# Optimization experiments

Hardware: AMD Instinct MI355X
Metric: run time of the kernel (lower is better)

Reference implementation:

```python
import jax, jax.numpy as jnp
import numpy as np

B, T, C, U = 256, 512, 512, 512  # batch, timesteps, n_in, units


def setup_inputs() -> dict:
    key = jax.random.key(0)
    k1, k2, k3, k4 = jax.random.split(key, 4)
    x = jax.random.normal(k1, (B, T, C), dtype=jnp.float32)
    dones = (jax.random.uniform(k2, (B, T, 1)) < 0.05).astype(jnp.float32)
    # keras 'uniform' initializer default range is [-0.05, 0.05]
    wx = jax.random.uniform(k3, (C, 4 * U), jnp.float32, -0.05, 0.05)
    wh = jax.random.uniform(k4, (U, 4 * U), jnp.float32, -0.05, 0.05)
    b = jnp.zeros((4 * U,), jnp.float32)
    return {"x": x, "dones": dones, "wx": wx, "wh": wh, "b": b}


def reference(x, dones, wx, wh, b):
    # x: [B,T,C], dones: [B,T,1], wx: [C,4U], wh: [U,4U], b: [4U]
    Bn, Tn, Cn = x.shape
    Un = wh.shape[0]

    def step(carry, xt):
        c, h = carry                     # [B,U] each
        xi, dt = xt                      # xi: [B,C], dt: [B,1]
        keep = 1.0 - dt
        c = c * keep
        h = h * keep
        z = xi @ wx + h @ wh + b         # [B,4U]
        i, f, o, u = jnp.split(z, 4, axis=-1)
        i = jax.nn.sigmoid(i)
        f = jax.nn.sigmoid(f)
        o = jax.nn.sigmoid(o)
        u = jnp.tanh(u)
        c = f * c + i * u
        h = o * jnp.tanh(c)
        return (c, h), h

    c0 = jnp.zeros((Bn, Un), x.dtype)   # self.states starts at zeros
    h0 = jnp.zeros((Bn, Un), x.dtype)
    (c, h), hs = jax.lax.scan(step, (c0, h0), (x.transpose(1, 0, 2), dones.transpose(1, 0, 2)))
    xs = hs.transpose(1, 0, 2)          # [B,T,U] (return_sequence=True)
    s = jnp.concatenate([c, h], axis=-1)  # [B,2U] (squeezed final state)
    return xs, s
```

## Files before the change

### kernel.cpp

```cpp
#include <hip/hip_runtime.h>

#define BATCH 256
#define TT 512
#define CIN 512
#define UU 512
#define ZN 2048
#define BT (BATCH*TT)
#define NWGPB 16

typedef __attribute__((ext_vector_type(8))) short short8;
typedef __attribute__((ext_vector_type(4))) float f32x4;

__device__ __forceinline__ short f2bf(float f){
  unsigned u = __float_as_uint(f);
  u += 0x7fffu + ((u >> 16) & 1u);
  return (short)(u >> 16);
}
__device__ __forceinline__ float bf2f(unsigned short s){
  unsigned u = ((unsigned)s) << 16;
  return __uint_as_float(u);
}

#define GLD16(g, l) __builtin_amdgcn_global_load_lds( \
    (const __attribute__((address_space(1))) void*)(g), \
    (__attribute__((address_space(3))) void*)(l), 16, 0, 0)

#define CLOAD(dst, p, OFFSTR) asm volatile( \
    "global_load_dwordx4 %0, %1, off offset:" OFFSTR " sc0 sc1" \
    : "=v"(dst) : "v"(p) : "memory")
#define CLOADW(dst, p) asm volatile( \
    "global_load_dword %0, %1, off sc0 sc1" \
    : "=v"(dst) : "v"(p) : "memory")

__device__ __forceinline__ void st_coh_u16(void* p, unsigned v){
  asm volatile("global_store_short %0, %1, off sc0 sc1" :: "v"(p), "v"(v) : "memory");
}
__device__ __forceinline__ void st_coh_u32(void* p, unsigned v){
  asm volatile("global_store_dword %0, %1, off sc0 sc1" :: "v"(p), "v"(v) : "memory");
}

__device__ __forceinline__ float sigm(float x){ return 1.0f/(1.0f + __expf(-x)); }
__device__ __forceinline__ float tanh_fast(float x){ return 1.0f - 2.0f/(1.0f + __expf(2.0f*x)); }

__global__ __launch_bounds__(256) void convert_x_kernel(const float* __restrict__ x,
                                                        short* __restrict__ xb){
  const long total = (long)TT*BATCH*64;
  const long stride = (long)gridDim.x * blockDim.x;
  for (long i = (long)blockIdx.x * blockDim.x + threadIdx.x; i < total; i += stride){
    const int c8 = (int)(i & 63);
    const long tb = i >> 6;
    const int b = (int)(tb & (BATCH-1));
    const int t = (int)(tb >> 8);
    const float* src = x + ((long)b*TT + t)*CIN + c8*8;
    const float4 v0 = *(const float4*)(src);
    const float4 v1 = *(const float4*)(src + 4);
    short8 o;
    o[0]=f2bf(v0.x); o[1]=f2bf(v0.y); o[2]=f2bf(v0.z); o[3]=f2bf(v0.w);
    o[4]=f2bf(v1.x); o[5]=f2bf(v1.y); o[6]=f2bf(v1.z); o[7]=f2bf(v1.w);
    *(short8*)(xb + i*8) = o;
  }
}

__global__ __launch_bounds__(256) void transpose_w_kernel(
    const float* __restrict__ wx, const float* __restrict__ wh,
    short* __restrict__ wxt, short* __restrict__ wht){
  const float* src = blockIdx.z ? wh : wx;
  short* dst = blockIdx.z ? wht : wxt;
  __shared__ float tile[32][33];
  const int nt = blockIdx.x << 5;
  const int kt = blockIdx.y << 5;
  const int tx = threadIdx.x & 31, ty = threadIdx.x >> 5;
  #pragma unroll
  for (int i = 0; i < 32; i += 8)
    tile[ty+i][tx] = src[(long)(kt+ty+i)*ZN + nt+tx];
  __syncthreads();
  #pragma unroll
  for (int i = 0; i < 32; i += 8)
    dst[(long)(nt+ty+i)*512 + kt+tx] = f2bf(tile[tx][ty+i]);
}

__global__ __launch_bounds__(256) void gemm_xpart_kernel(
    const short* __restrict__ A, const short* __restrict__ Bt,
    const float* __restrict__ bias, short* __restrict__ Co){
  __shared__ short As[128*32];
  __shared__ short Bs[128*32];
  const int wg = blockIdx.x;
  const int xcd = wg & 7;
  const int ii = wg >> 3;
  const long m0 = (long)(xcd*128 + (ii >> 4)) << 7;
  const long n0 = (long)(ii & 15) << 7;
  const int tid = threadIdx.x;
  const int lane = tid & 63;
  const int wave = tid >> 6;
  const int wm = wave & 1, wn = wave >> 1;
  f32x4 acc[4][4] = {};
  const int srow = tid >> 2;
  const int sseg = tid & 3;
  const long aoff = (m0 + srow) * 512 + sseg * 8;
  const long boff = (n0 + srow) * 512 + sseg * 8;
  short* ldsa = &As[tid * 8];
  short* ldsb = &Bs[tid * 8];
  for (int k0 = 0; k0 < 512; k0 += 32){
    __syncthreads();
    GLD16(A + aoff + k0, ldsa);
    GLD16(A + aoff + 64*512 + k0, ldsa + 2048);
    GLD16(Bt + boff + k0, ldsb);
    GLD16(Bt + boff + 64*512 + k0, ldsb + 2048);
    __syncthreads();
    const int kb = (lane >> 4) * 8;
    short8 af[4], bf[4];
    #pragma unroll
    for (int mi = 0; mi < 4; mi++) af[mi] = *(const short8*)&As[(wm*64 + mi*16 + (lane&15))*32 + kb];
    #pragma unroll
    for (int ni = 0; ni < 4; ni++) bf[ni] = *(const short8*)&Bs[(wn*64 + ni*16 + (lane&15))*32 + kb];
    #pragma unroll
    for (int mi = 0; mi < 4; mi++)
      #pragma unroll
      for (int ni = 0; ni < 4; ni++)
        acc[mi][ni] = __builtin_amdgcn_mfma_f32_16x16x32_bf16(af[mi], bf[ni], acc[mi][ni], 0, 0, 0);
  }
  #pragma unroll
  for (int ni = 0; ni < 4; ni++){
    const long col = n0 + wn*64 + ni*16 + (lane & 15);
    const float bv = bias[col];
    #pragma unroll
    for (int mi = 0; mi < 4; mi++){
      const long row = m0 + wm*64 + mi*16 + ((lane >> 4) << 2);
      #pragma unroll
      for (int r = 0; r < 4; r++)
        Co[(row + r)*ZN + col] = f2bf(acc[mi][ni][r] + bv);
    }
  }
}

__global__ __launch_bounds__(512, 2) void lstm_persist_kernel(
    const short* __restrict__ xpart, const float* __restrict__ dones,
    const short* __restrict__ wht, short* __restrict__ hb0,
    short* __restrict__ hb1, unsigned* __restrict__ flags,
    float* __restrict__ out){
  __shared__ short h_lds[8192];
  __shared__ float zpart[128*19 + 16];
  const int tid = threadIdx.x;
  const int lane = tid & 63;
  const int wv = tid >> 6;
  const int bg = blockIdx.x & 15;
  const int cg = blockIdx.x >> 4;
  const int rb = bg << 4;
  const int uc = cg << 5;
  const int j = lane & 15;
  const int hq = lane >> 4;
  const int g_w = wv >> 1;
  const int ucl = ((wv & 1) << 4) + j;
  const int zl = g_w*32 + ucl;

  short8 bfr[16];
  {
    const short* wsrc = wht + ((long)(g_w*512 + uc + ucl))*512 + hq*8;
    #pragma unroll
    for (int m = 0; m < 16; m++)
      bfr[m] = *(const short8*)(wsrc + m*32);
  }

  const int srow = tid >> 5;
  const int scol = (tid & 31) << 4;
  const int swb = (srow << 10) + (scol << 1);
  const int sxor = (srow & 7) << 4;
  const int arb = (j << 10) + (hq << 4);
  const int axor = (j & 7) << 4;

  const int erow = tid >> 5;
  const int euj  = tid & 31;
  const int eucol = uc + euj;
  const int row  = rb + erow;

  unsigned* fl = flags + bg*16;
  const unsigned short* xp16 = (const unsigned short*)xpart;

  float c = 0.0f;
  float dn;
  unsigned short xp[4];
  dn = dones[(long)row*TT + 0];
  #pragma unroll
  for (int g = 0; g < 4; g++)
    xp[g] = xp16[((long)0*BATCH + row)*ZN + (g<<9) + eucol];

  for (int t = 0; t < TT; t++){
    {
      const short* hsrc = ((t & 1) ? hb1 : hb0) + (long)(rb + srow)*UU + scol;
      short8 hv0, hv1;
      CLOAD(hv0, hsrc, "0");
      CLOAD(hv1, hsrc, "16");
      asm volatile("s_waitcnt vmcnt(0)" ::: "memory");
      *(short8*)((char*)h_lds + ( swb       ^ sxor)) = hv0;
      *(short8*)((char*)h_lds + ((swb + 16) ^ sxor)) = hv1;
    }
    __syncthreads();
    short8 a[16];
    #pragma unroll
    for (int m = 0; m < 16; m++)
      a[m] = *(const short8*)((const char*)h_lds + ((arb + (m << 6)) ^ axor));
    f32x4 acc0 = {}, acc1 = {};
    #pragma unroll
    for (int m = 0; m < 16; m += 2){
      acc0 = __builtin_amdgcn_mfma_f32_16x16x32_bf16(a[m],   bfr[m],   acc0, 0, 0, 0);
      acc1 = __builtin_amdgcn_mfma_f32_16x16x32_bf16(a[m+1], bfr[m+1], acc1, 0, 0, 0);
    }
    const f32x4 acc = acc0 + acc1;
    #pragma unroll
    for (int r = 0; r < 4; r++)
      zpart[zl*19 + hq*4 + r] = acc[r];
    __syncthreads();
    const float keep = 1.0f - dn;
    const float cold = c * keep;
    const float z0 = bf2f(xp[0]) + keep*zpart[(0*32 + euj)*19 + erow];
    const float z1 = bf2f(xp[1]) + keep*zpart[(1*32 + euj)*19 + erow];
    const float z2 = bf2f(xp[2]) + keep*zpart[(2*32 + euj)*19 + erow];
    const float z3 = bf2f(xp[3]) + keep*zpart[(3*32 + euj)*19 + erow];
    const float gi = sigm(z0);
    const float gf = sigm(z1);
    const float go = sigm(z2);
    const float gu = tanh_fast(z3);
    const float cn = gf*cold + gi*gu;
    const float hn = go * tanh_fast(cn);
    c = cn;
    if (t == TT-1){
      out[(long)row*TT*UU + (long)t*UU + eucol] = hn;
      float* s = out + (long)BATCH*TT*UU;
      s[(long)row*2*UU + eucol] = cn;
      s[(long)row*2*UU + UU + eucol] = hn;
    } else {
      short* hdst = (t & 1) ? hb0 : hb1;
      st_coh_u16(hdst + (long)row*UU + eucol, (unsigned)(unsigned short)f2bf(hn));
      asm volatile("s_waitcnt vmcnt(0)" ::: "memory");
      __syncthreads();
      if (tid == 0) st_coh_u32(fl + cg, (unsigned)(t+1));
      out[(long)row*TT*UU + (long)t*UU + eucol] = hn;
      dn = dones[(long)row*TT + (t+1)];
      #pragma unroll
      for (int g = 0; g < 4; g++)
        xp[g] = xp16[((long)(t+1)*BATCH + row)*ZN + (g<<9) + eucol];
      if (wv == 0){
        const unsigned tgt = (unsigned)(t+1);
        unsigned v;
        for (;;){
          CLOADW(v, fl + (lane & 15));
          asm volatile("s_waitcnt vmcnt(0)" ::: "memory");
          if (__all((int)(v >= tgt))) break;
          __builtin_amdgcn_s_sleep(1);
        }
      }
      __syncthreads();
    }
  }
}

extern "C" void kernel_launch(void* const* d_in, const int* in_sizes, int n_in,
                              void* d_out, int out_size, void* d_ws, size_t ws_size,
                              hipStream_t stream){
  const float* x     = (const float*)d_in[0];
  const float* dones = (const float*)d_in[1];
  const float* wx    = (const float*)d_in[2];
  const float* wh    = (const float*)d_in[3];
  const float* b     = (const float*)d_in[4];
  float* out = (float*)d_out;
  char* ws = (char*)d_ws;
  short* x_tb  = (short*)(ws);
  short* wx_t  = (short*)(ws + 134217728L);
  short* wh_t  = (short*)(ws + 136314880L);
  short* xpart = (short*)(ws + 138412032L);
  short* hb0   = (short*)(ws + 675282944L);
  short* hb1   = (short*)(ws + 675545088L);
  unsigned* flags = (unsigned*)(ws + 675807232L);

  hipMemsetAsync(hb0, 0, 262144, stream);
  hipMemsetAsync(flags, 0, 1024, stream);
  convert_x_kernel<<<2048, 256, 0, stream>>>(x, x_tb);
  transpose_w_kernel<<<dim3(64,16,2), 256, 0, stream>>>(wx, wh, wx_t, wh_t);
  gemm_xpart_kernel<<<16384, 256, 0, stream>>>(x_tb, wx_t, b, xpart);
  lstm_persist_kernel<<<256, 512, 0, stream>>>(xpart, dones, wh_t, hb0, hb1, flags, out);
}
```

Measured before the change: 1.856 ms.

## Restructure persistent LSTM step to 4 waves with split-K and per-gate MFMA reuse

The recurrent kernel drops from 512 to 256 threads per workgroup. Each wave now holds weights for all four gates of 16 units over half of K, and reuses each loaded h fragment across four MFMAs. Partial sums from the K halves are exchanged through LDS, and each lane computes the cell update for two rows directly from its accumulators, so the padded transposed zpart shuffle is gone. This cuts LDS reads and the number of waves that sync per step, at the cost of more weight registers per thread and an unswizzled LDS layout that may cause bank conflicts.

```diff
diff --git a/kernel.cpp b/kernel.cpp
--- a/kernel.cpp
+++ b/kernel.cpp
@@ -6,7 +6,6 @@
 #define UU 512
 #define ZN 2048
 #define BT (BATCH*TT)
-#define NWGPB 16
 
 typedef __attribute__((ext_vector_type(8))) short short8;
 typedef __attribute__((ext_vector_type(4))) float f32x4;
@@ -133,117 +132,140 @@
   }
 }
 
-__global__ __launch_bounds__(512, 2) void lstm_persist_kernel(
+__global__ __launch_bounds__(256, 1) void lstm_persist_kernel(
     const short* __restrict__ xpart, const float* __restrict__ dones,
     const short* __restrict__ wht, short* __restrict__ hb0,
     short* __restrict__ hb1, unsigned* __restrict__ flags,
     float* __restrict__ out){
   __shared__ short h_lds[8192];
-  __shared__ float zpart[128*19 + 16];
+  __shared__ float zx[4096];
   const int tid = threadIdx.x;
-  const int lane = tid & 63;
+  const int l = tid & 63;
   const int wv = tid >> 6;
+  const int kh = wv & 1;
+  const int ug = wv >> 1;
   const int bg = blockIdx.x & 15;
   const int cg = blockIdx.x >> 4;
   const int rb = bg << 4;
-  const int uc = cg << 5;
-  const int j = lane & 15;
-  const int hq = lane >> 4;
-  const int g_w = wv >> 1;
-  const int ucl = ((wv & 1) << 4) + j;
-  const int zl = g_w*32 + ucl;
-
-  short8 bfr[16];
-  {
-    const short* wsrc = wht + ((long)(g_w*512 + uc + ucl))*512 + hq*8;
-    #pragma unroll
-    for (int m = 0; m < 16; m++)
-      bfr[m] = *(const short8*)(wsrc + m*32);
-  }
-
-  const int srow = tid >> 5;
-  const int scol = (tid & 31) << 4;
-  const int swb = (srow << 10) + (scol << 1);
-  const int sxor = (srow & 7) << 4;
-  const int arb = (j << 10) + (hq << 4);
-  const int axor = (j & 7) << 4;
-
-  const int erow = tid >> 5;
-  const int euj  = tid & 31;
-  const int eucol = uc + euj;
-  const int row  = rb + erow;
+  const int ucw = (cg << 5) + (ug << 4);
+  const int j = l & 15;
+  const int hq = l >> 4;
+
+  short8 bfr[4][8];
+  #pragma unroll
+  for (int g = 0; g < 4; g++){
+    const short* wsrc = wht + ((long)(g*512 + ucw + j))*512 + kh*256 + hq*8;
+    #pragma unroll
+    for (int m = 0; m < 8; m++)
+      bfr[g][m] = *(const short8*)(wsrc + m*32);
+  }
+
+  const int srow = tid & 15;
+  const int skg  = tid >> 4;
+  const long sgoff = (long)(rb + srow)*UU + skg*32;
+  short* sdst = h_lds + skg*512 + srow*8;
+
+  const int row0 = rb + hq*4 + kh*2;
+  const int ucol = ucw + j;
 
   unsigned* fl = flags + bg*16;
   const unsigned short* xp16 = (const unsigned short*)xpart;
 
-  float c = 0.0f;
-  float dn;
-  unsigned short xp[4];
-  dn = dones[(long)row*TT + 0];
-  #pragma unroll
-  for (int g = 0; g < 4; g++)
-    xp[g] = xp16[((long)0*BATCH + row)*ZN + (g<<9) + eucol];
+  float c0 = 0.f, c1 = 0.f;
+  float dn0, dn1;
+  unsigned short xp0[4], xp1[4];
+  dn0 = dones[(long)row0*TT];
+  dn1 = dones[(long)(row0+1)*TT];
+  #pragma unroll
+  for (int g = 0; g < 4; g++){
+    xp0[g] = xp16[(long)row0*ZN + (g<<9) + ucol];
+    xp1[g] = xp16[(long)(row0+1)*ZN + (g<<9) + ucol];
+  }
 
   for (int t = 0; t < TT; t++){
     {
-      const short* hsrc = ((t & 1) ? hb1 : hb0) + (long)(rb + srow)*UU + scol;
-      short8 hv0, hv1;
-      CLOAD(hv0, hsrc, "0");
-      CLOAD(hv1, hsrc, "16");
+      const short* hs = ((t & 1) ? hb1 : hb0) + sgoff;
+      short8 v0, v1, v2, v3;
+      CLOAD(v0, hs, "0"); CLOAD(v1, hs, "16"); CLOAD(v2, hs, "32"); CLOAD(v3, hs, "48");
       asm volatile("s_waitcnt vmcnt(0)" ::: "memory");
-      *(short8*)((char*)h_lds + ( swb       ^ sxor)) = hv0;
-      *(short8*)((char*)h_lds + ((swb + 16) ^ sxor)) = hv1;
+      *(short8*)(sdst      ) = v0;
+      *(short8*)(sdst + 128) = v1;
+      *(short8*)(sdst + 256) = v2;
+      *(short8*)(sdst + 384) = v3;
     }
     __syncthreads();
-    short8 a[16];
-    #pragma unroll
-    for (int m = 0; m < 16; m++)
-      a[m] = *(const short8*)((const char*)h_lds + ((arb + (m << 6)) ^ axor));
-    f32x4 acc0 = {}, acc1 = {};
-    #pragma unroll
-    for (int m = 0; m < 16; m += 2){
-      acc0 = __builtin_amdgcn_mfma_f32_16x16x32_bf16(a[m],   bfr[m],   acc0, 0, 0, 0);
-      acc1 = __builtin_amdgcn_mfma_f32_16x16x32_bf16(a[m+1], bfr[m+1], acc1, 0, 0, 0);
-    }
-    const f32x4 acc = acc0 + acc1;
-    #pragma unroll
-    for (int r = 0; r < 4; r++)
-      zpart[zl*19 + hq*4 + r] = acc[r];
+    f32x4 acc[4] = {};
+    const short* abase = h_lds + kh*4096 + l*8;
+    #pragma unroll
+    for (int m = 0; m < 8; m++){
+      const short8 a = *(const short8*)(abase + m*512);
+      #pragma unroll
+      for (int g = 0; g < 4; g++)
+        acc[g] = __builtin_amdgcn_mfma_f32_16x16x32_bf16(a, bfr[g][m], acc[g], 0, 0, 0);
+    }
+    #pragma unroll
+    for (int g = 0; g < 4; g++)
+      *(f32x4*)&zx[(wv*4 + g)*256 + l*4] = acc[g];
     __syncthreads();
-    const float keep = 1.0f - dn;
-    const float cold = c * keep;
-    const float z0 = bf2f(xp[0]) + keep*zpart[(0*32 + euj)*19 + erow];
-    const float z1 = bf2f(xp[1]) + keep*zpart[(1*32 + euj)*19 + erow];
-    const float z2 = bf2f(xp[2]) + keep*zpart[(2*32 + euj)*19 + erow];
-    const float z3 = bf2f(xp[3]) + keep*zpart[(3*32 + euj)*19 + erow];
-    const float gi = sigm(z0);
-    const float gf = sigm(z1);
-    const float go = sigm(z2);
-    const float gu = tanh_fast(z3);
-    const float cn = gf*cold + gi*gu;
-    const float hn = go * tanh_fast(cn);
-    c = cn;
+    const int pvb = (wv ^ 1)*4;
+    f32x4 pz[4];
+    #pragma unroll
+    for (int g = 0; g < 4; g++)
+      pz[g] = *(const f32x4*)&zx[(pvb + g)*256 + l*4];
+    float zs0[4], zs1[4];
+    #pragma unroll
+    for (int g = 0; g < 4; g++){
+      zs0[g] = kh ? (acc[g][2] + pz[g][2]) : (acc[g][0] + pz[g][0]);
+      zs1[g] = kh ? (acc[g][3] + pz[g][3]) : (acc[g][1] + pz[g][1]);
+    }
+    const float keep0 = 1.0f - dn0;
+    const float keep1 = 1.0f - dn1;
+    const float z00 = bf2f(xp0[0]) + keep0*zs0[0];
+    const float z01 = bf2f(xp0[1]) + keep0*zs0[1];
+    const float z02 = bf2f(xp0[2]) + keep0*zs0[2];
+    const float z03 = bf2f(xp0[3]) + keep0*zs0[3];
+    const float z10 = bf2f(xp1[0]) + keep1*zs1[0];
+    const float z11 = bf2f(xp1[1]) + keep1*zs1[1];
+    const float z12 = bf2f(xp1[2]) + keep1*zs1[2];
+    const float z13 = bf2f(xp1[3]) + keep1*zs1[3];
+    const float gi0 = sigm(z00), gf0 = sigm(z01), go0 = sigm(z02), gu0 = tanh_fast(z03);
+    const float gi1 = sigm(z10), gf1 = sigm(z11), go1 = sigm(z12), gu1 = tanh_fast(z13);
+    const float cn0 = gf0*(c0*keep0) + gi0*gu0;
+    const float cn1 = gf1*(c1*keep1) + gi1*gu1;
+    const float hn0 = go0 * tanh_fast(cn0);
+    const float hn1 = go1 * tanh_fast(cn1);
+    c0 = cn0; c1 = cn1;
+    const long ob0 = (long)row0*TT*UU + (long)t*UU + ucol;
     if (t == TT-1){
-      out[(long)row*TT*UU + (long)t*UU + eucol] = hn;
+      out[ob0] = hn0;
+      out[ob0 + (long)TT*UU] = hn1;
       float* s = out + (long)BATCH*TT*UU;
-      s[(long)row*2*UU + eucol] = cn;
-      s[(long)row*2*UU + UU + eucol] = hn;
+      s[(long)row0*2*UU + ucol] = cn0;
+      s[(long)row0*2*UU + UU + ucol] = hn0;
+      s[(long)(row0+1)*2*UU + ucol] = cn1;
+      s[(long)(row0+1)*2*UU + UU + ucol] = hn1;
     } else {
       short* hdst = (t & 1) ? hb0 : hb1;
-      st_coh_u16(hdst + (long)row*UU + eucol, (unsigned)(unsigned short)f2bf(hn));
+      st_coh_u16(hdst + (long)row0*UU + ucol, (unsigned)(unsigned short)f2bf(hn0));
+      st_coh_u16(hdst + (long)(row0+1)*UU + ucol, (unsigned)(unsigned short)f2bf(hn1));
       asm volatile("s_waitcnt vmcnt(0)" ::: "memory");
       __syncthreads();
       if (tid == 0) st_coh_u32(fl + cg, (unsigned)(t+1));
-      out[(long)row*TT*UU + (long)t*UU + eucol] = hn;
-      dn = dones[(long)row*TT + (t+1)];
+      out[ob0] = hn0;
+      out[ob0 + (long)TT*UU] = hn1;
+      dn0 = dones[(long)row0*TT + (t+1)];
+      dn1 = dones[(long)(row0+1)*TT + (t+1)];
+      const long xb = ((long)(t+1)*BATCH)*ZN + ucol;
       #pragma unroll
-      for (int g = 0; g < 4; g++)
-        xp[g] = xp16[((long)(t+1)*BATCH + row)*ZN + (g<<9) + eucol];
+      for (int g = 0; g < 4; g++){
+        xp0[g] = xp16[xb + (long)row0*ZN + (g<<9)];
+        xp1[g] = xp16[xb + (long)(row0+1)*ZN + (g<<9)];
+      }
       if (wv == 0){
         const unsigned tgt = (unsigned)(t+1);
         unsigned v;
         for (;;){
-          CLOADW(v, fl + (lane & 15));
+          CLOADW(v, fl + (l & 15));
           asm volatile("s_waitcnt vmcnt(0)" ::: "memory");
           if (__all((int)(v >= tgt))) break;
           __builtin_amdgcn_s_sleep(1);
@@ -277,5 +299,5 @@
   convert_x_kernel<<<2048, 256, 0, stream>>>(x, x_tb);
   transpose_w_kernel<<<dim3(64,16,2), 256, 0, stream>>>(wx, wh, wx_t, wh_t);
   gemm_xpart_kernel<<<16384, 256, 0, stream>>>(x_tb, wx_t, b, xpart);
-  lstm_persist_kernel<<<256, 512, 0, stream>>>(xpart, dones, wh_t, hb0, hb1, flags, out);
-}
+  lstm_persist_kernel<<<256, 256, 0, stream>>>(xpart, dones, wh_t, hb0, hb1, flags, out);
+}
```

After: 2.076 ms. +11.8%, slower.

## Split persistent LSTM across 512 smaller workgroups with 16-unit column slices

Applied to the files above, without the earlier changes.

Repartitions the persistent recurrent kernel from 256 workgroups of 512 threads (32 units each) to 512 workgroups of 256 threads (16 units each), so each batch group now synchronizes 32 workgroups instead of 16. The LDS layout for h is changed to a k-major, unswizzled arrangement that lets lanes read MFMA A-fragments directly, and the register prefetch of all 16 fragments is replaced with on-the-fly loads. This spreads the per-step work across more CUs to shorten the serial step latency, at the cost of a wider flag barrier, each block re-loading the full 16-row h tile for less compute, and possible LDS bank conflicts without the XOR swizzle.

```diff
diff --git a/kernel.cpp b/kernel.cpp
--- a/kernel.cpp
+++ b/kernel.cpp
@@ -6,7 +6,6 @@
 #define UU 512
 #define ZN 2048
 #define BT (BATCH*TT)
-#define NWGPB 16
 
 typedef __attribute__((ext_vector_type(8))) short short8;
 typedef __attribute__((ext_vector_type(4))) float f32x4;
@@ -133,89 +132,85 @@
   }
 }
 
-__global__ __launch_bounds__(512, 2) void lstm_persist_kernel(
+__global__ __launch_bounds__(256, 2) void lstm_persist_kernel(
     const short* __restrict__ xpart, const float* __restrict__ dones,
     const short* __restrict__ wht, short* __restrict__ hb0,
     short* __restrict__ hb1, unsigned* __restrict__ flags,
     float* __restrict__ out){
   __shared__ short h_lds[8192];
-  __shared__ float zpart[128*19 + 16];
+  __shared__ float zpart[64*19 + 16];
   const int tid = threadIdx.x;
-  const int lane = tid & 63;
+  const int l = tid & 63;
   const int wv = tid >> 6;
-  const int bg = blockIdx.x & 15;
-  const int cg = blockIdx.x >> 4;
+  const int bg = blockIdx.x >> 5;
+  const int cg = blockIdx.x & 31;
   const int rb = bg << 4;
-  const int uc = cg << 5;
-  const int j = lane & 15;
-  const int hq = lane >> 4;
-  const int g_w = wv >> 1;
-  const int ucl = ((wv & 1) << 4) + j;
-  const int zl = g_w*32 + ucl;
+  const int uc = cg << 4;
+  const int j = l & 15;
+  const int hq = l >> 4;
 
   short8 bfr[16];
   {
-    const short* wsrc = wht + ((long)(g_w*512 + uc + ucl))*512 + hq*8;
+    const short* wsrc = wht + ((long)(wv*512 + uc + j))*512 + hq*8;
     #pragma unroll
     for (int m = 0; m < 16; m++)
       bfr[m] = *(const short8*)(wsrc + m*32);
   }
 
-  const int srow = tid >> 5;
-  const int scol = (tid & 31) << 4;
-  const int swb = (srow << 10) + (scol << 1);
-  const int sxor = (srow & 7) << 4;
-  const int arb = (j << 10) + (hq << 4);
-  const int axor = (j & 7) << 4;
-
-  const int erow = tid >> 5;
-  const int euj  = tid & 31;
+  const int srow = tid & 15;
+  const int skg  = tid >> 4;
+  const long sgoff = (long)(rb + srow)*UU + skg*32;
+  short* sdst = h_lds + skg*512 + srow*8;
+
+  const int erow = tid >> 4;
+  const int euj  = tid & 15;
   const int eucol = uc + euj;
   const int row  = rb + erow;
 
-  unsigned* fl = flags + bg*16;
+  unsigned* fl = flags + bg*32;
   const unsigned short* xp16 = (const unsigned short*)xpart;
 
   float c = 0.0f;
   float dn;
   unsigned short xp[4];
-  dn = dones[(long)row*TT + 0];
+  dn = dones[(long)row*TT];
   #pragma unroll
   for (int g = 0; g < 4; g++)
-    xp[g] = xp16[((long)0*BATCH + row)*ZN + (g<<9) + eucol];
+    xp[g] = xp16[(long)row*ZN + (g<<9) + eucol];
 
   for (int t = 0; t < TT; t++){
     {
-      const short* hsrc = ((t & 1) ? hb1 : hb0) + (long)(rb + srow)*UU + scol;
-      short8 hv0, hv1;
-      CLOAD(hv0, hsrc, "0");
-      CLOAD(hv1, hsrc, "16");
+      const short* hs = ((t & 1) ? hb1 : hb0) + sgoff;
+      short8 v0, v1, v2, v3;
+      CLOAD(v0, hs, "0"); CLOAD(v1, hs, "16"); CLOAD(v2, hs, "32"); CLOAD(v3, hs, "48");
       asm volatile("s_waitcnt vmcnt(0)" ::: "memory");
-      *(short8*)((char*)h_lds + ( swb       ^ sxor)) = hv0;
-      *(short8*)((char*)h_lds + ((swb + 16) ^ sxor)) = hv1;
-    }
-    __syncthreads();
-    short8 a[16];
-    #pragma unroll
-    for (int m = 0; m < 16; m++)
-      a[m] = *(const short8*)((const char*)h_lds + ((arb + (m << 6)) ^ axor));
+      *(short8*)(sdst      ) = v0;
+      *(short8*)(sdst + 128) = v1;
+      *(short8*)(sdst + 256) = v2;
+      *(short8*)(sdst + 384) = v3;
+    }
+    __syncthreads();
+    const short* abase = h_lds + l*8;
     f32x4 acc0 = {}, acc1 = {};
     #pragma unroll
     for (int m = 0; m < 16; m += 2){
-      acc0 = __builtin_amdgcn_mfma_f32_16x16x32_bf16(a[m],   bfr[m],   acc0, 0, 0, 0);
-      acc1 = __builtin_amdgcn_mfma_f32_16x16x32_bf16(a[m+1], bfr[m+1], acc1, 0, 0, 0);
+      const short8 a0 = *(const short8*)(abase + m*512);
+      const short8 a1 = *(const short8*)(abase + m*512 + 512);
+      acc0 = __builtin_amdgcn_mfma_f32_16x16x32_bf16(a0, bfr[m],   acc0, 0, 0, 0);
+      acc1 = __builtin_amdgcn_mfma_f32_16x16x32_bf16(a1, bfr[m+1], acc1, 0, 0, 0);
     }
     const f32x4 acc = acc0 + acc1;
+    const int zl = wv*16 + j;
     #pragma unroll
     for (int r = 0; r < 4; r++)
       zpart[zl*19 + hq*4 + r] = acc[r];
     __syncthreads();
     const float keep = 1.0f - dn;
     const float cold = c * keep;
-    const float z0 = bf2f(xp[0]) + keep*zpart[(0*32 + euj)*19 + erow];
-    const float z1 = bf2f(xp[1]) + keep*zpart[(1*32 + euj)*19 + erow];
-    const float z2 = bf2f(xp[2]) + keep*zpart[(2*32 + euj)*19 + erow];
-    const float z3 = bf2f(xp[3]) + keep*zpart[(3*32 + euj)*19 + erow];
+    const float z0 = bf2f(xp[0]) + keep*zpart[(0*16 + euj)*19 + erow];
+    const float z1 = bf2f(xp[1]) + keep*zpart[(1*16 + euj)*19 + erow];
+    const float z2 = bf2f(xp[2]) + keep*zpart[(2*16 + euj)*19 + erow];
+    const float z3 = bf2f(xp[3]) + keep*zpart[(3*16 + euj)*19 + erow];
     const float gi = sigm(z0);
     const float gf = sigm(z1);
     const float go = sigm(z2);
@@ -236,14 +231,15 @@
       if (tid == 0) st_coh_u32(fl + cg, (unsigned)(t+1));
       out[(long)row*TT*UU + (long)t*UU + eucol] = hn;
       dn = dones[(long)row*TT + (t+1)];
+      const long xb = ((long)(t+1)*BATCH + row)*ZN + eucol;
       #pragma unroll
       for (int g = 0; g < 4; g++)
-        xp[g] = xp16[((long)(t+1)*BATCH + row)*ZN + (g<<9) + eucol];
+        xp[g] = xp16[xb + (g<<9)];
       if (wv == 0){
         const unsigned tgt = (unsigned)(t+1);
         unsigned v;
         for (;;){
-          CLOADW(v, fl + (lane & 15));
+          CLOADW(v, fl + (l & 31));
           asm volatile("s_waitcnt vmcnt(0)" ::: "memory");
           if (__all((int)(v >= tgt))) break;
           __builtin_amdgcn_s_sleep(1);
@@ -273,9 +269,9 @@
   unsigned* flags = (unsigned*)(ws + 675807232L);
 
   hipMemsetAsync(hb0, 0, 262144, stream);
-  hipMemsetAsync(flags, 0, 1024, stream);
+  hipMemsetAsync(flags, 0, 2048, stream);
   convert_x_kernel<<<2048, 256, 0, stream>>>(x, x_tb);
   transpose_w_kernel<<<dim3(64,16,2), 256, 0, stream>>>(wx, wh, wx_t, wh_t);
   gemm_xpart_kernel<<<16384, 256, 0, stream>>>(x_tb, wx_t, b, xpart);
-  lstm_persist_kernel<<<256, 512, 0, stream>>>(xpart, dones, wh_t, hb0, hb1, flags, out);
-}
+  lstm_persist_kernel<<<512, 256, 0, stream>>>(xpart, dones, wh_t, hb0, hb1, flags, out);
+}
```

Measured after the change: 2.715 ms. +46.3%, slower.

## Fuse x fp32-to-bf16 conversion into input GEMM and simplify h LDS layout

Applied to the files above, without the earlier changes.

Removes the separate convert_x kernel and has the input-projection GEMM read fp32 x directly, converting to bf16 while staging into LDS, which drops one full pass over x and the bf16 intermediate buffer. The GEMM's A-tile loads change from async global-to-LDS copies to register loads plus explicit LDS stores, which may add latency per k-step. The persistent LSTM kernel also reorganizes how h is staged in LDS so each lane reads its MFMA fragment with a simple linear offset, without the XOR swizzle and the up-front register array.

```diff
diff --git a/kernel.cpp b/kernel.cpp
--- a/kernel.cpp
+++ b/kernel.cpp
@@ -6,7 +6,6 @@
 #define UU 512
 #define ZN 2048
 #define BT (BATCH*TT)
-#define NWGPB 16
 
 typedef __attribute__((ext_vector_type(8))) short short8;
 typedef __attribute__((ext_vector_type(4))) float f32x4;
@@ -41,25 +40,6 @@
 
 __device__ __forceinline__ float sigm(float x){ return 1.0f/(1.0f + __expf(-x)); }
 __device__ __forceinline__ float tanh_fast(float x){ return 1.0f - 2.0f/(1.0f + __expf(2.0f*x)); }
-
-__global__ __launch_bounds__(256) void convert_x_kernel(const float* __restrict__ x,
-                                                        short* __restrict__ xb){
-  const long total = (long)TT*BATCH*64;
-  const long stride = (long)gridDim.x * blockDim.x;
-  for (long i = (long)blockIdx.x * blockDim.x + threadIdx.x; i < total; i += stride){
-    const int c8 = (int)(i & 63);
-    const long tb = i >> 6;
-    const int b = (int)(tb & (BATCH-1));
-    const int t = (int)(tb >> 8);
-    const float* src = x + ((long)b*TT + t)*CIN + c8*8;
-    const float4 v0 = *(const float4*)(src);
-    const float4 v1 = *(const float4*)(src + 4);
-    short8 o;
-    o[0]=f2bf(v0.x); o[1]=f2bf(v0.y); o[2]=f2bf(v0.z); o[3]=f2bf(v0.w);
-    o[4]=f2bf(v1.x); o[5]=f2bf(v1.y); o[6]=f2bf(v1.z); o[7]=f2bf(v1.w);
-    *(short8*)(xb + i*8) = o;
-  }
-}
 
 __global__ __launch_bounds__(256) void transpose_w_kernel(
     const float* __restrict__ wx, const float* __restrict__ wh,
@@ -80,7 +60,7 @@
 }
 
 __global__ __launch_bounds__(256) void gemm_xpart_kernel(
-    const short* __restrict__ A, const short* __restrict__ Bt,
+    const float* __restrict__ x, const short* __restrict__ Bt,
     const float* __restrict__ bias, short* __restrict__ Co){
   __shared__ short As[128*32];
   __shared__ short Bs[128*32];
@@ -96,16 +76,28 @@
   f32x4 acc[4][4] = {};
   const int srow = tid >> 2;
   const int sseg = tid & 3;
-  const long aoff = (m0 + srow) * 512 + sseg * 8;
+  const long mA = m0 + srow;
+  const long mB2 = m0 + srow + 64;
+  const float* aptrA = x + ((long)(mA  & 255)*TT + (mA  >> 8))*CIN + sseg*8;
+  const float* aptrB = x + ((long)(mB2 & 255)*TT + (mB2 >> 8))*CIN + sseg*8;
   const long boff = (n0 + srow) * 512 + sseg * 8;
   short* ldsa = &As[tid * 8];
   short* ldsb = &Bs[tid * 8];
   for (int k0 = 0; k0 < 512; k0 += 32){
     __syncthreads();
-    GLD16(A + aoff + k0, ldsa);
-    GLD16(A + aoff + 64*512 + k0, ldsa + 2048);
     GLD16(Bt + boff + k0, ldsb);
     GLD16(Bt + boff + 64*512 + k0, ldsb + 2048);
+    const float4 a0 = *(const float4*)(aptrA + k0);
+    const float4 a1 = *(const float4*)(aptrA + k0 + 4);
+    const float4 b0 = *(const float4*)(aptrB + k0);
+    const float4 b1 = *(const float4*)(aptrB + k0 + 4);
+    short8 sa, sb;
+    sa[0]=f2bf(a0.x); sa[1]=f2bf(a0.y); sa[2]=f2bf(a0.z); sa[3]=f2bf(a0.w);
+    sa[4]=f2bf(a1.x); sa[5]=f2bf(a1.y); sa[6]=f2bf(a1.z); sa[7]=f2bf(a1.w);
+    sb[0]=f2bf(b0.x); sb[1]=f2bf(b0.y); sb[2]=f2bf(b0.z); sb[3]=f2bf(b0.w);
+    sb[4]=f2bf(b1.x); sb[5]=f2bf(b1.y); sb[6]=f2bf(b1.z); sb[7]=f2bf(b1.w);
+    *(short8*)ldsa = sa;
+    *(short8*)(ldsa + 2048) = sb;
     __syncthreads();
     const int kb = (lane >> 4) * 8;
     short8 af[4], bf[4];
@@ -161,12 +153,10 @@
       bfr[m] = *(const short8*)(wsrc + m*32);
   }
 
-  const int srow = tid >> 5;
-  const int scol = (tid & 31) << 4;
-  const int swb = (srow << 10) + (scol << 1);
-  const int sxor = (srow & 7) << 4;
-  const int arb = (j << 10) + (hq << 4);
-  const int axor = (j & 7) << 4;
+  const int srow = tid & 15;
+  const int skg  = tid >> 4;
+  const long sgoff = (long)(rb + srow)*UU + skg*16;
+  short* sdst = h_lds + skg*256 + srow*8;
 
   const int erow = tid >> 5;
   const int euj  = tid & 31;
@@ -179,31 +169,29 @@
   float c = 0.0f;
   float dn;
   unsigned short xp[4];
-  dn = dones[(long)row*TT + 0];
+  dn = dones[(long)row*TT];
   #pragma unroll
   for (int g = 0; g < 4; g++)
-    xp[g] = xp16[((long)0*BATCH + row)*ZN + (g<<9) + eucol];
+    xp[g] = xp16[(long)row*ZN + (g<<9) + eucol];
 
   for (int t = 0; t < TT; t++){
     {
-      const short* hsrc = ((t & 1) ? hb1 : hb0) + (long)(rb + srow)*UU + scol;
-      short8 hv0, hv1;
-      CLOAD(hv0, hsrc, "0");
-      CLOAD(hv1, hsrc, "16");
+      const short* hs = ((t & 1) ? hb1 : hb0) + sgoff;
+      short8 v0, v1;
+      CLOAD(v0, hs, "0"); CLOAD(v1, hs, "16");
       asm volatile("s_waitcnt vmcnt(0)" ::: "memory");
-      *(short8*)((char*)h_lds + ( swb       ^ sxor)) = hv0;
-      *(short8*)((char*)h_lds + ((swb + 16) ^ sxor)) = hv1;
-    }
-    __syncthreads();
-    short8 a[16];
-    #pragma unroll
-    for (int m = 0; m < 16; m++)
-      a[m] = *(const short8*)((const char*)h_lds + ((arb + (m << 6)) ^ axor));
+      *(short8*)(sdst      ) = v0;
+      *(short8*)(sdst + 128) = v1;
+    }
+    __syncthreads();
+    const short* abase = h_lds + lane*8;
     f32x4 acc0 = {}, acc1 = {};
     #pragma unroll
     for (int m = 0; m < 16; m += 2){
-      acc0 = __builtin_amdgcn_mfma_f32_16x16x32_bf16(a[m],   bfr[m],   acc0, 0, 0, 0);
-      acc1 = __builtin_amdgcn_mfma_f32_16x16x32_bf16(a[m+1], bfr[m+1], acc1, 0, 0, 0);
+      const short8 a0 = *(const short8*)(abase + m*512);
+      const short8 a1 = *(const short8*)(abase + m*512 + 512);
+      acc0 = __builtin_amdgcn_mfma_f32_16x16x32_bf16(a0, bfr[m],   acc0, 0, 0, 0);
+      acc1 = __builtin_amdgcn_mfma_f32_16x16x32_bf16(a1, bfr[m+1], acc1, 0, 0, 0);
     }
     const f32x4 acc = acc0 + acc1;
     #pragma unroll
@@ -236,9 +224,10 @@
       if (tid == 0) st_coh_u32(fl + cg, (unsigned)(t+1));
       out[(long)row*TT*UU + (long)t*UU + eucol] = hn;
       dn = dones[(long)row*TT + (t+1)];
+      const long xb = ((long)(t+1)*BATCH + row)*ZN + eucol;
       #pragma unroll
       for (int g = 0; g < 4; g++)
-        xp[g] = xp16[((long)(t+1)*BATCH + row)*ZN + (g<<9) + eucol];
+        xp[g] = xp16[xb + (g<<9)];
       if (wv == 0){
         const unsigned tgt = (unsigned)(t+1);
         unsigned v;
@@ -264,18 +253,16 @@
   const float* b     = (const float*)d_in[4];
   float* out = (float*)d_out;
   char* ws = (char*)d_ws;
-  short* x_tb  = (short*)(ws);
-  short* wx_t  = (short*)(ws + 134217728L);
-  short* wh_t  = (short*)(ws + 136314880L);
-  short* xpart = (short*)(ws + 138412032L);
-  short* hb0   = (short*)(ws + 675282944L);
-  short* hb1   = (short*)(ws + 675545088L);
-  unsigned* flags = (unsigned*)(ws + 675807232L);
+  short* xpart = (short*)(ws);
+  short* wx_t  = (short*)(ws + 536870912L);
+  short* wh_t  = (short*)(ws + 538968064L);
+  short* hb0   = (short*)(ws + 541065216L);
+  short* hb1   = (short*)(ws + 541327360L);
+  unsigned* flags = (unsigned*)(ws + 541589504L);
 
   hipMemsetAsync(hb0, 0, 262144, stream);
   hipMemsetAsync(flags, 0, 1024, stream);
-  convert_x_kernel<<<2048, 256, 0, stream>>>(x, x_tb);
   transpose_w_kernel<<<dim3(64,16,2), 256, 0, stream>>>(wx, wh, wx_t, wh_t);
-  gemm_xpart_kernel<<<16384, 256, 0, stream>>>(x_tb, wx_t, b, xpart);
+  gemm_xpart_kernel<<<16384, 256, 0, stream>>>(x, wx_t, b, xpart);
   lstm_persist_kernel<<<256, 512, 0, stream>>>(xpart, dones, wh_t, hb0, hb1, flags, out);
 }
```

After: 2.009 ms. 1.08x slower.
